# Kernel optimization log

Measured on AMD Instinct MI355X. Metric: run time of the kernel, lower is better.

## Reference

```python
import jax, jax.numpy as jnp
import numpy as np

N_NODES = 100000
N_EDGES = 1700000
NFEAT, NHID1, NHID2, NCLASS = 256, 128, 64, 200


def _deg_inv_sqrt(idx, n):
    deg = jax.ops.segment_sum(jnp.ones(idx.shape[0], jnp.float32), idx, num_segments=n)
    return jnp.power(jnp.clip(deg, 1.0), -0.5)


def _graph_conv(x, W, b, src, dst, n):
    # DGL GraphConv norm='both': D_out^{-1/2} A D_in^{-1/2} X W + b
    # transform first (in_feats >= out_feats), then normalized aggregation
    h = x @ W                                   # [N, out]
    h = h * _deg_inv_sqrt(src, n)[:, None]      # source (out-degree) norm
    m = jax.ops.segment_sum(h[src], dst, num_segments=n)  # SpMM aggregate
    m = m * _deg_inv_sqrt(dst, n)[:, None]      # dest (in-degree) norm
    return m + b


def setup_inputs() -> dict:
    key = jax.random.key(0)
    ks = jax.random.split(key, 9)
    x = jax.random.normal(ks[0], (N_NODES, NFEAT), jnp.float32)
    src = jax.random.randint(ks[1], (N_EDGES,), 0, N_NODES, jnp.int64)
    dst = jax.random.randint(ks[2], (N_EDGES,), 0, N_NODES, jnp.int64)
    def glorot(k, fan_in, fan_out):
        s = jnp.sqrt(6.0 / (fan_in + fan_out))
        return jax.random.uniform(k, (fan_in, fan_out), jnp.float32, -s, s)
    return {
        "x": x, "src": src, "dst": dst,
        "W1": glorot(ks[3], NFEAT, NHID1), "b1": jnp.zeros((NHID1,), jnp.float32),
        "W2": glorot(ks[4], NHID1, NHID2), "b2": jnp.zeros((NHID2,), jnp.float32),
        "Wf": glorot(ks[5], NHID2, NCLASS), "bf": jnp.zeros((NCLASS,), jnp.float32),
    }


def reference(x, src, dst, W1, b1, W2, b2, Wf, bf):
    n = x.shape[0]
    h = jax.nn.relu(_graph_conv(x, W1, b1, src, dst, n))
    # dropout is identity in eval mode (training=False)
    h = jax.nn.relu(_graph_conv(h, W2, b2, src, dst, n))
    logits = h @ Wf + bf
    return jax.nn.log_softmax(logits, axis=1)
```

## Files before the change

kernel.cpp:

```cpp
#include <hip/hip_runtime.h>
#include <math.h>

#define N_NODES 100000
#define N_EDGES 1700000
#define F0 256
#define F1 128
#define F2 64
#define NCLS 200
#define NFPAD 208
#define CAP 64

typedef short bf16x8 __attribute__((ext_vector_type(8)));
typedef float f32x4 __attribute__((ext_vector_type(4)));

__device__ __forceinline__ unsigned short f2bf(float f) {
  unsigned u = __float_as_uint(f);
  return (unsigned short)((u + 0x7FFFu + ((u >> 16) & 1u)) >> 16);
}
__device__ __forceinline__ float bflo(unsigned u) { return __uint_as_float(u << 16); }
__device__ __forceinline__ float bfhi(unsigned u) { return __uint_as_float(u & 0xFFFF0000u); }

__global__ __launch_bounds__(256) void k_dinv(const unsigned* __restrict__ cs,
                                              const unsigned* __restrict__ cnt,
                                              float* __restrict__ dsrc,
                                              float* __restrict__ ddst) {
  int i = blockIdx.x * 256 + threadIdx.x;
  if (i < N_NODES) {
    dsrc[i] = rsqrtf((float)max(cs[i], 1u));
    ddst[i] = rsqrtf((float)max(cnt[i], 1u));
  }
}

__global__ __launch_bounds__(256) void k_castw(const float* __restrict__ W,
                                               unsigned short* __restrict__ Wt,
                                               int K, int N) {
  int idx = blockIdx.x * 256 + threadIdx.x;
  if (idx < K * N) {
    int n = idx / K, k = idx % K;
    Wt[idx] = f2bf(W[(size_t)k * N + n]);
  }
}

__global__ __launch_bounds__(256) void k_castwf(const float* __restrict__ Wf,
                                                unsigned short* __restrict__ Wfp) {
  int idx = blockIdx.x * 256 + threadIdx.x;
  if (idx < NFPAD * F2) {
    int n = idx / F2, k = idx % F2;
    Wfp[idx] = (n < NCLS) ? f2bf(Wf[(size_t)k * NCLS + n]) : (unsigned short)0;
  }
}

__global__ __launch_bounds__(256) void k_fill_gemm1(const int* __restrict__ src,
                                                    const int* __restrict__ dst,
                                                    unsigned* __restrict__ cs,
                                                    unsigned* __restrict__ cnt,
                                                    int* __restrict__ bucket,
                                                    const float* __restrict__ X,
                                                    const unsigned short* __restrict__ Wt,
                                                    unsigned short* __restrict__ out) {
  constexpr int BM = 128;
  constexpr int BK = 64;
  constexpr int LDR = BK + 8;
  constexpr int NB_GEMM = (N_NODES + BM - 1) / BM;
  constexpr int NB_FILL = 2048;
  constexpr int TOT = NB_GEMM + NB_FILL;

  __shared__ unsigned short as[BM][LDR];
  __shared__ unsigned short bs[F1][LDR];

  const int bid = blockIdx.x;
  const int g0 = (int)(((long long)bid * NB_GEMM) / TOT);
  const int g1 = (int)(((long long)(bid + 1) * NB_GEMM) / TOT);

  if (g1 > g0) {
    const int tid = threadIdx.x;
    const int lane = tid & 63;
    const int wid = tid >> 6;
    const int wr = wid >> 1;
    const int wc = wid & 1;
    const int row0 = wr * 64;
    const int col0 = wc * 64;
    const int fq = lane >> 4;
    const int fr = lane & 15;
    const int brow0 = g0 * BM;

    f32x4 acc[4][4];
#pragma unroll
    for (int m = 0; m < 4; ++m)
#pragma unroll
      for (int n = 0; n < 4; ++n) acc[m][n] = (f32x4)(0.f);

    for (int k0 = 0; k0 < F0; k0 += BK) {
      __syncthreads();
      for (int chunk = tid; chunk < BM * (BK / 8); chunk += 256) {
        int r = chunk >> 3, c = chunk & 7;
        int gr = brow0 + r;
        float4 v0 = make_float4(0.f, 0.f, 0.f, 0.f), v1 = v0;
        if (gr < N_NODES) {
          const float* p = X + (size_t)gr * F0 + k0 + c * 8;
          v0 = *(const float4*)p;
          v1 = *(const float4*)(p + 4);
        }
        bf16x8 o;
        o[0] = (short)f2bf(v0.x); o[1] = (short)f2bf(v0.y);
        o[2] = (short)f2bf(v0.z); o[3] = (short)f2bf(v0.w);
        o[4] = (short)f2bf(v1.x); o[5] = (short)f2bf(v1.y);
        o[6] = (short)f2bf(v1.z); o[7] = (short)f2bf(v1.w);
        *(bf16x8*)&as[r][c * 8] = o;
      }
      for (int chunk = tid; chunk < F1 * (BK / 8); chunk += 256) {
        int r = chunk >> 3, c = chunk & 7;
        *(uint4*)&bs[r][c * 8] = *(const uint4*)(Wt + (size_t)r * F0 + k0 + c * 8);
      }
      __syncthreads();
#pragma unroll
      for (int ks = 0; ks < 2; ++ks) {
        bf16x8 af[4], bfv[4];
#pragma unroll
        for (int m = 0; m < 4; ++m)
          af[m] = *(const bf16x8*)&as[row0 + m * 16 + fr][ks * 32 + fq * 8];
#pragma unroll
        for (int n = 0; n < 4; ++n)
          bfv[n] = *(const bf16x8*)&bs[col0 + n * 16 + fr][ks * 32 + fq * 8];
#pragma unroll
        for (int m = 0; m < 4; ++m)
#pragma unroll
          for (int n = 0; n < 4; ++n)
            acc[m][n] = __builtin_amdgcn_mfma_f32_16x16x32_bf16(af[m], bfv[n], acc[m][n], 0, 0, 0);
      }
    }
#pragma unroll
    for (int m = 0; m < 4; ++m) {
#pragma unroll
      for (int j = 0; j < 4; ++j) {
        int grow = brow0 + row0 + m * 16 + fq * 4 + j;
        if (grow < N_NODES) {
#pragma unroll
          for (int n = 0; n < 4; ++n) {
            int col = col0 + n * 16 + fr;
            out[(size_t)grow * F1 + col] = f2bf(acc[m][n][j]);
          }
        }
      }
    }
  } else {
    const int fb = bid - g0;
    int i = fb * 256 + threadIdx.x;
    for (int e = i; e < N_EDGES; e += NB_FILL * 256) {
      int s = src[e], d = dst[e];
      unsigned p = atomicAdd(&cnt[d], 1u);
      if (p < CAP) bucket[d * CAP + p] = s;
      atomicAdd(&cs[s], 1u);
    }
  }
}

template <int K, int BN>
__global__ void k_gemm_mfma(const unsigned short* __restrict__ X,
                            const unsigned short* __restrict__ Wt,
                            const float* __restrict__ scale,
                            unsigned short* __restrict__ out) {
  constexpr int BM = 128;
  constexpr int BK = 64;
  constexpr int LDR = BK + 8;
  constexpr int NWAVE = 2 * (BN / 64);
  constexpr int NTHR = NWAVE * 64;
  __shared__ unsigned short as[BM][LDR];
  __shared__ unsigned short bs[BN][LDR];

  const int tid = threadIdx.x;
  const int lane = tid & 63;
  const int wid = tid >> 6;
  constexpr int WCOLS = BN / 64;
  const int wr = wid / WCOLS;
  const int wc = wid % WCOLS;
  const int row0 = wr * 64;
  const int col0 = wc * 64;
  const int fq = lane >> 4;
  const int fr = lane & 15;
  const int brow0 = blockIdx.x * BM;

  f32x4 acc[4][4];
#pragma unroll
  for (int m = 0; m < 4; ++m)
#pragma unroll
    for (int n = 0; n < 4; ++n) acc[m][n] = (f32x4)(0.f);

  for (int k0 = 0; k0 < K; k0 += BK) {
    __syncthreads();
    for (int chunk = tid; chunk < BM * (BK / 8); chunk += NTHR) {
      int r = chunk >> 3, c = chunk & 7;
      int gr = brow0 + r;
      uint4 v = make_uint4(0u, 0u, 0u, 0u);
      if (gr < N_NODES) v = *(const uint4*)(X + (size_t)gr * K + k0 + c * 8);
      *(uint4*)&as[r][c * 8] = v;
    }
    for (int chunk = tid; chunk < BN * (BK / 8); chunk += NTHR) {
      int r = chunk >> 3, c = chunk & 7;
      *(uint4*)&bs[r][c * 8] = *(const uint4*)(Wt + (size_t)r * K + k0 + c * 8);
    }
    __syncthreads();
#pragma unroll
    for (int ks = 0; ks < 2; ++ks) {
      bf16x8 af[4], bfv[4];
#pragma unroll
      for (int m = 0; m < 4; ++m)
        af[m] = *(const bf16x8*)&as[row0 + m * 16 + fr][ks * 32 + fq * 8];
#pragma unroll
      for (int n = 0; n < 4; ++n)
        bfv[n] = *(const bf16x8*)&bs[col0 + n * 16 + fr][ks * 32 + fq * 8];
#pragma unroll
      for (int m = 0; m < 4; ++m)
#pragma unroll
        for (int n = 0; n < 4; ++n)
          acc[m][n] = __builtin_amdgcn_mfma_f32_16x16x32_bf16(af[m], bfv[n], acc[m][n], 0, 0, 0);
    }
  }

#pragma unroll
  for (int m = 0; m < 4; ++m) {
#pragma unroll
    for (int j = 0; j < 4; ++j) {
      int grow = brow0 + row0 + m * 16 + fq * 4 + j;
      if (grow < N_NODES) {
        float sc = scale[grow];
#pragma unroll
        for (int n = 0; n < 4; ++n) {
          int col = col0 + n * 16 + fr;
          out[(size_t)grow * BN + col] = f2bf(acc[m][n][j] * sc);
        }
      }
    }
  }
}

__global__ __launch_bounds__(256) void k_gather128(const int* __restrict__ bucket,
                                                   const unsigned* __restrict__ cnt,
                                                   const unsigned short* __restrict__ h,
                                                   const float* __restrict__ dsrc,
                                                   const float* __restrict__ ddst,
                                                   const float* __restrict__ b,
                                                   unsigned short* __restrict__ out) {
  const int lane = threadIdx.x & 63;
  const int node = blockIdx.x * 4 + (threadIdx.x >> 6);
  if (node >= N_NODES) return;
  const unsigned deg = min(cnt[node], (unsigned)CAP);
  const int* bp = bucket + (size_t)node * CAP;
  int bidx = (lane < (int)deg) ? bp[lane] : 0;
  float dsv = dsrc[bidx];
  const unsigned* hp = (const unsigned*)h;
  float a0 = 0.f, a1 = 0.f;
  int j = 0;
  for (; j + 4 <= (int)deg; j += 4) {
    int s0 = __shfl(bidx, j + 0), s1 = __shfl(bidx, j + 1);
    int s2 = __shfl(bidx, j + 2), s3 = __shfl(bidx, j + 3);
    float d0 = __shfl(dsv, j + 0), d1 = __shfl(dsv, j + 1);
    float d2 = __shfl(dsv, j + 2), d3 = __shfl(dsv, j + 3);
    unsigned u0 = hp[(size_t)s0 * 64 + lane];
    unsigned u1 = hp[(size_t)s1 * 64 + lane];
    unsigned u2 = hp[(size_t)s2 * 64 + lane];
    unsigned u3 = hp[(size_t)s3 * 64 + lane];
    a0 += d0 * bflo(u0) + d1 * bflo(u1) + d2 * bflo(u2) + d3 * bflo(u3);
    a1 += d0 * bfhi(u0) + d1 * bfhi(u1) + d2 * bfhi(u2) + d3 * bfhi(u3);
  }
  for (; j < (int)deg; ++j) {
    int s = __shfl(bidx, j);
    float ds = __shfl(dsv, j);
    unsigned u = hp[(size_t)s * 64 + lane];
    a0 += ds * bflo(u);
    a1 += ds * bfhi(u);
  }
  float dd = ddst[node];
  float2 bb = *(const float2*)(b + lane * 2);
  float v0 = fmaxf(a0 * dd + bb.x, 0.f);
  float v1 = fmaxf(a1 * dd + bb.y, 0.f);
  unsigned o = (unsigned)f2bf(v0) | ((unsigned)f2bf(v1) << 16);
  ((unsigned*)out)[(size_t)node * 64 + lane] = o;
}

__global__ __launch_bounds__(256) void k_gather64(const int* __restrict__ bucket,
                                                  const unsigned* __restrict__ cnt,
                                                  const unsigned short* __restrict__ h,
                                                  const float* __restrict__ ddst,
                                                  const float* __restrict__ b,
                                                  unsigned short* __restrict__ out) {
  const int lane = threadIdx.x & 63;
  const int node = blockIdx.x * 4 + (threadIdx.x >> 6);
  if (node >= N_NODES) return;
  const int half = lane >> 5;
  const int fl = lane & 31;
  const unsigned deg = min(cnt[node], (unsigned)CAP);
  const int* bp = bucket + (size_t)node * CAP;
  int bidx = (lane < (int)deg) ? bp[lane] : 0;
  const unsigned* hp = (const unsigned*)h;
  float a0 = 0.f, a1 = 0.f;
  int j = half;
  for (; j + 2 < (int)deg; j += 4) {
    int s0 = __shfl(bidx, j), s1 = __shfl(bidx, j + 2);
    unsigned u0 = hp[(size_t)s0 * 32 + fl];
    unsigned u1 = hp[(size_t)s1 * 32 + fl];
    a0 += bflo(u0) + bflo(u1);
    a1 += bfhi(u0) + bfhi(u1);
  }
  if (j < (int)deg) {
    int s = __shfl(bidx, j);
    unsigned u = hp[(size_t)s * 32 + fl];
    a0 += bflo(u);
    a1 += bfhi(u);
  }
  a0 += __shfl_xor(a0, 32);
  a1 += __shfl_xor(a1, 32);
  if (half == 0) {
    float dd = ddst[node];
    float2 bb = *(const float2*)(b + fl * 2);
    float v0 = fmaxf(a0 * dd + bb.x, 0.f);
    float v1 = fmaxf(a1 * dd + bb.y, 0.f);
    unsigned o = (unsigned)f2bf(v0) | ((unsigned)f2bf(v1) << 16);
    ((unsigned*)out)[(size_t)node * 32 + fl] = o;
  }
}

__global__ __launch_bounds__(256) void k_final_mfma(const unsigned short* __restrict__ h,
                                                    const unsigned short* __restrict__ Wfp,
                                                    const float* __restrict__ bf,
                                                    float* __restrict__ out) {
  constexpr int BM = 64;
  constexpr int NF = NFPAD / 16;
  constexpr int LDR = F2 + 8;
  __shared__ unsigned short as[BM][LDR];
  __shared__ unsigned short bs[NFPAD][LDR];

  const int tid = threadIdx.x;
  const int lane = tid & 63;
  const int wid = tid >> 6;
  const int fq = lane >> 4;
  const int fr = lane & 15;
  const int brow0 = blockIdx.x * BM;

  for (int chunk = tid; chunk < BM * 8; chunk += 256) {
    int r = chunk >> 3, c = chunk & 7;
    int gr = brow0 + r;
    uint4 v = make_uint4(0u, 0u, 0u, 0u);
    if (gr < N_NODES) v = *(const uint4*)(h + (size_t)gr * F2 + c * 8);
    *(uint4*)&as[r][c * 8] = v;
  }
  for (int chunk = tid; chunk < NFPAD * 8; chunk += 256) {
    int r = chunk >> 3, c = chunk & 7;
    *(uint4*)&bs[r][c * 8] = *(const uint4*)(Wfp + (size_t)r * F2 + c * 8);
  }
  __syncthreads();

  f32x4 acc[NF];
#pragma unroll
  for (int n = 0; n < NF; ++n) acc[n] = (f32x4)(0.f);

#pragma unroll
  for (int ks = 0; ks < 2; ++ks) {
    bf16x8 af = *(const bf16x8*)&as[wid * 16 + fr][ks * 32 + fq * 8];
#pragma unroll
    for (int n = 0; n < NF; ++n) {
      bf16x8 bv = *(const bf16x8*)&bs[n * 16 + fr][ks * 32 + fq * 8];
      acc[n] = __builtin_amdgcn_mfma_f32_16x16x32_bf16(af, bv, acc[n], 0, 0, 0);
    }
  }

  const int nval = (fr < NCLS - (NF - 1) * 16) ? NF : NF - 1;
  float bias[NF];
#pragma unroll
  for (int n = 0; n < NF; ++n) {
    int col = n * 16 + fr;
    bias[n] = (col < NCLS) ? bf[col] : 0.f;
  }

#pragma unroll
  for (int j = 0; j < 4; ++j) {
    const int grow = brow0 + wid * 16 + fq * 4 + j;
    float v[NF];
    float m = -1e30f;
#pragma unroll
    for (int n = 0; n < NF; ++n) {
      v[n] = acc[n][j] + bias[n];
      if (n < nval) m = fmaxf(m, v[n]);
    }
#pragma unroll
    for (int o = 1; o < 16; o <<= 1) m = fmaxf(m, __shfl_xor(m, o));
    float s = 0.f;
#pragma unroll
    for (int n = 0; n < NF; ++n)
      if (n < nval) s += expf(v[n] - m);
#pragma unroll
    for (int o = 1; o < 16; o <<= 1) s += __shfl_xor(s, o);
    float ls = logf(s);
    if (grow < N_NODES) {
#pragma unroll
      for (int n = 0; n < NF; ++n)
        if (n < nval) out[(size_t)grow * NCLS + n * 16 + fr] = v[n] - m - ls;
    }
  }
}

extern "C" void kernel_launch(void* const* d_in, const int* in_sizes, int n_in,
                              void* d_out, int out_size, void* d_ws, size_t ws_size,
                              hipStream_t stream) {
  const float* x = (const float*)d_in[0];
  const int* src = (const int*)d_in[1];
  const int* dst = (const int*)d_in[2];
  const float* W1 = (const float*)d_in[3];
  const float* b1 = (const float*)d_in[4];
  const float* W2 = (const float*)d_in[5];
  const float* b2 = (const float*)d_in[6];
  const float* Wf = (const float*)d_in[7];
  const float* bf = (const float*)d_in[8];
  float* out = (float*)d_out;

  char* base = (char*)d_ws;
  size_t off = 0;
  auto alloc = [&](size_t bytes) -> void* {
    off = (off + 255) & ~(size_t)255;
    void* p = base + off;
    off += bytes;
    return p;
  };
  unsigned* cs = (unsigned*)alloc(2 * (size_t)N_NODES * 4);
  unsigned* cnt = cs + N_NODES;
  float* dsrc = (float*)alloc(N_NODES * 4);
  float* ddst = (float*)alloc(N_NODES * 4);
  int* bucket = (int*)alloc((size_t)N_NODES * CAP * 4);
  unsigned short* P1 = (unsigned short*)alloc((size_t)N_NODES * F1 * 2);
  unsigned short* P2 = (unsigned short*)alloc((size_t)N_NODES * F1 * 2);
  unsigned short* wt1 = (unsigned short*)alloc((size_t)F1 * F0 * 2);
  unsigned short* wt2 = (unsigned short*)alloc((size_t)F2 * F1 * 2);
  unsigned short* wtf = (unsigned short*)alloc((size_t)NFPAD * F2 * 2);

  unsigned short* h1 = P1;
  unsigned short* h1f = P2;
  unsigned short* h2 = P1;
  unsigned short* agg2 = P2;

  hipMemsetAsync(cs, 0, 2 * (size_t)N_NODES * sizeof(unsigned), stream);

  k_castw<<<(F0 * F1 + 255) / 256, 256, 0, stream>>>(W1, wt1, F0, F1);
  k_castw<<<(F1 * F2 + 255) / 256, 256, 0, stream>>>(W2, wt2, F1, F2);
  k_castwf<<<(NFPAD * F2 + 255) / 256, 256, 0, stream>>>(Wf, wtf);

  constexpr int NB_GEMM = (N_NODES + 127) / 128;
  constexpr int NB_FILL = 2048;
  k_fill_gemm1<<<NB_GEMM + NB_FILL, 256, 0, stream>>>(src, dst, cs, cnt, bucket, x, wt1, h1);

  k_dinv<<<(N_NODES + 255) / 256, 256, 0, stream>>>(cs, cnt, dsrc, ddst);

  k_gather128<<<(N_NODES + 3) / 4, 256, 0, stream>>>(bucket, cnt, h1, dsrc, ddst, b1, h1f);

  k_gemm_mfma<F1, F2><<<(N_NODES + 127) / 128, 128, 0, stream>>>(h1f, wt2, dsrc, h2);
  k_gather64<<<(N_NODES + 3) / 4, 256, 0, stream>>>(bucket, cnt, h2, ddst, b2, agg2);

  k_final_mfma<<<(N_NODES + 63) / 64, 256, 0, stream>>>(agg2, wtf, bf, out);
}
```

Baseline: 340.7 us.

## Merge weight casts, inline degree normalization, and retile layer-2 GEMM

Folds the three weight-cast kernels into one launch and drops the separate degree inverse-sqrt kernel. The gathers and the layer-2 GEMM now compute rsqrt of the raw counts inline. The layer-2 GEMM is replaced by a dedicated kernel with 64-row tiles and two waves, which doubles the block count for better occupancy. This removes two launches and the dsrc/ddst arrays, at the cost of recomputing rsqrt per neighbor and per row, and of a smaller tile with less weight reuse.

```diff
diff --git a/kernel.cpp b/kernel.cpp
--- a/kernel.cpp
+++ b/kernel.cpp
@@ -20,33 +20,24 @@
 __device__ __forceinline__ float bflo(unsigned u) { return __uint_as_float(u << 16); }
 __device__ __forceinline__ float bfhi(unsigned u) { return __uint_as_float(u & 0xFFFF0000u); }
 
-__global__ __launch_bounds__(256) void k_dinv(const unsigned* __restrict__ cs,
-                                              const unsigned* __restrict__ cnt,
-                                              float* __restrict__ dsrc,
-                                              float* __restrict__ ddst) {
-  int i = blockIdx.x * 256 + threadIdx.x;
-  if (i < N_NODES) {
-    dsrc[i] = rsqrtf((float)max(cs[i], 1u));
-    ddst[i] = rsqrtf((float)max(cnt[i], 1u));
-  }
-}
-
-__global__ __launch_bounds__(256) void k_castw(const float* __restrict__ W,
-                                               unsigned short* __restrict__ Wt,
-                                               int K, int N) {
+__global__ __launch_bounds__(256) void k_castall(const float* __restrict__ W1,
+                                                 const float* __restrict__ W2,
+                                                 const float* __restrict__ Wf,
+                                                 unsigned short* __restrict__ wt1,
+                                                 unsigned short* __restrict__ wt2,
+                                                 unsigned short* __restrict__ wtf) {
   int idx = blockIdx.x * 256 + threadIdx.x;
-  if (idx < K * N) {
-    int n = idx / K, k = idx % K;
-    Wt[idx] = f2bf(W[(size_t)k * N + n]);
-  }
-}
-
-__global__ __launch_bounds__(256) void k_castwf(const float* __restrict__ Wf,
-                                                unsigned short* __restrict__ Wfp) {
-  int idx = blockIdx.x * 256 + threadIdx.x;
-  if (idx < NFPAD * F2) {
-    int n = idx / F2, k = idx % F2;
-    Wfp[idx] = (n < NCLS) ? f2bf(Wf[(size_t)k * NCLS + n]) : (unsigned short)0;
+  if (idx < F1 * F0) {
+    int n = idx / F0, k = idx % F0;
+    wt1[idx] = f2bf(W1[(size_t)k * F1 + n]);
+  } else if (idx < F1 * F0 + F2 * F1) {
+    int t = idx - F1 * F0;
+    int n = t / F1, k = t % F1;
+    wt2[t] = f2bf(W2[(size_t)k * F2 + n]);
+  } else if (idx < F1 * F0 + F2 * F1 + NFPAD * F2) {
+    int t = idx - F1 * F0 - F2 * F1;
+    int n = t / F2, k = t % F2;
+    wtf[t] = (n < NCLS) ? f2bf(Wf[(size_t)k * NCLS + n]) : (unsigned short)0;
   }
 }
 
@@ -155,103 +146,24 @@
   }
 }
 
-template <int K, int BN>
-__global__ void k_gemm_mfma(const unsigned short* __restrict__ X,
-                            const unsigned short* __restrict__ Wt,
-                            const float* __restrict__ scale,
-                            unsigned short* __restrict__ out) {
-  constexpr int BM = 128;
-  constexpr int BK = 64;
-  constexpr int LDR = BK + 8;
-  constexpr int NWAVE = 2 * (BN / 64);
-  constexpr int NTHR = NWAVE * 64;
-  __shared__ unsigned short as[BM][LDR];
-  __shared__ unsigned short bs[BN][LDR];
-
-  const int tid = threadIdx.x;
-  const int lane = tid & 63;
-  const int wid = tid >> 6;
-  constexpr int WCOLS = BN / 64;
-  const int wr = wid / WCOLS;
-  const int wc = wid % WCOLS;
-  const int row0 = wr * 64;
-  const int col0 = wc * 64;
-  const int fq = lane >> 4;
-  const int fr = lane & 15;
-  const int brow0 = blockIdx.x * BM;
-
-  f32x4 acc[4][4];
-#pragma unroll
-  for (int m = 0; m < 4; ++m)
-#pragma unroll
-    for (int n = 0; n < 4; ++n) acc[m][n] = (f32x4)(0.f);
-
-  for (int k0 = 0; k0 < K; k0 += BK) {
-    __syncthreads();
-    for (int chunk = tid; chunk < BM * (BK / 8); chunk += NTHR) {
-      int r = chunk >> 3, c = chunk & 7;
-      int gr = brow0 + r;
-      uint4 v = make_uint4(0u, 0u, 0u, 0u);
-      if (gr < N_NODES) v = *(const uint4*)(X + (size_t)gr * K + k0 + c * 8);
-      *(uint4*)&as[r][c * 8] = v;
-    }
-    for (int chunk = tid; chunk < BN * (BK / 8); chunk += NTHR) {
-      int r = chunk >> 3, c = chunk & 7;
-      *(uint4*)&bs[r][c * 8] = *(const uint4*)(Wt + (size_t)r * K + k0 + c * 8);
-    }
-    __syncthreads();
-#pragma unroll
-    for (int ks = 0; ks < 2; ++ks) {
-      bf16x8 af[4], bfv[4];
-#pragma unroll
-      for (int m = 0; m < 4; ++m)
-        af[m] = *(const bf16x8*)&as[row0 + m * 16 + fr][ks * 32 + fq * 8];
-#pragma unroll
-      for (int n = 0; n < 4; ++n)
-        bfv[n] = *(const bf16x8*)&bs[col0 + n * 16 + fr][ks * 32 + fq * 8];
-#pragma unroll
-      for (int m = 0; m < 4; ++m)
-#pragma unroll
-        for (int n = 0; n < 4; ++n)
-          acc[m][n] = __builtin_amdgcn_mfma_f32_16x16x32_bf16(af[m], bfv[n], acc[m][n], 0, 0, 0);
-    }
-  }
-
-#pragma unroll
-  for (int m = 0; m < 4; ++m) {
-#pragma unroll
-    for (int j = 0; j < 4; ++j) {
-      int grow = brow0 + row0 + m * 16 + fq * 4 + j;
-      if (grow < N_NODES) {
-        float sc = scale[grow];
-#pragma unroll
-        for (int n = 0; n < 4; ++n) {
-          int col = col0 + n * 16 + fr;
-          out[(size_t)grow * BN + col] = f2bf(acc[m][n][j] * sc);
-        }
-      }
-    }
-  }
-}
-
 __global__ __launch_bounds__(256) void k_gather128(const int* __restrict__ bucket,
+                                                   const unsigned* __restrict__ cs,
                                                    const unsigned* __restrict__ cnt,
                                                    const unsigned short* __restrict__ h,
-                                                   const float* __restrict__ dsrc,
-                                                   const float* __restrict__ ddst,
                                                    const float* __restrict__ b,
                                                    unsigned short* __restrict__ out) {
   const int lane = threadIdx.x & 63;
   const int node = blockIdx.x * 4 + (threadIdx.x >> 6);
   if (node >= N_NODES) return;
-  const unsigned deg = min(cnt[node], (unsigned)CAP);
+  const unsigned craw = cnt[node];
+  const int deg = (int)min(craw, (unsigned)CAP);
   const int* bp = bucket + (size_t)node * CAP;
-  int bidx = (lane < (int)deg) ? bp[lane] : 0;
-  float dsv = dsrc[bidx];
+  int bidx = (lane < deg) ? bp[lane] : 0;
+  float dsv = rsqrtf((float)max(cs[bidx], 1u));
   const unsigned* hp = (const unsigned*)h;
   float a0 = 0.f, a1 = 0.f;
   int j = 0;
-  for (; j + 4 <= (int)deg; j += 4) {
+  for (; j + 4 <= deg; j += 4) {
     int s0 = __shfl(bidx, j + 0), s1 = __shfl(bidx, j + 1);
     int s2 = __shfl(bidx, j + 2), s3 = __shfl(bidx, j + 3);
     float d0 = __shfl(dsv, j + 0), d1 = __shfl(dsv, j + 1);
@@ -263,14 +175,14 @@
     a0 += d0 * bflo(u0) + d1 * bflo(u1) + d2 * bflo(u2) + d3 * bflo(u3);
     a1 += d0 * bfhi(u0) + d1 * bfhi(u1) + d2 * bfhi(u2) + d3 * bfhi(u3);
   }
-  for (; j < (int)deg; ++j) {
+  for (; j < deg; ++j) {
     int s = __shfl(bidx, j);
     float ds = __shfl(dsv, j);
     unsigned u = hp[(size_t)s * 64 + lane];
     a0 += ds * bflo(u);
     a1 += ds * bfhi(u);
   }
-  float dd = ddst[node];
+  float dd = rsqrtf((float)max(craw, 1u));
   float2 bb = *(const float2*)(b + lane * 2);
   float v0 = fmaxf(a0 * dd + bb.x, 0.f);
   float v1 = fmaxf(a1 * dd + bb.y, 0.f);
@@ -278,10 +190,81 @@
   ((unsigned*)out)[(size_t)node * 64 + lane] = o;
 }
 
+__global__ __launch_bounds__(128) void k_gemm2(const unsigned short* __restrict__ X,
+                                               const unsigned short* __restrict__ Wt,
+                                               const unsigned* __restrict__ cs,
+                                               unsigned short* __restrict__ out) {
+  constexpr int BM = 64;
+  constexpr int BK = 64;
+  constexpr int LDR = BK + 8;
+  __shared__ unsigned short as[BM][LDR];
+  __shared__ unsigned short bs[F2][LDR];
+
+  const int tid = threadIdx.x;
+  const int lane = tid & 63;
+  const int wid = tid >> 6;
+  const int row0 = wid * 32;
+  const int fq = lane >> 4;
+  const int fr = lane & 15;
+  const int brow0 = blockIdx.x * BM;
+
+  f32x4 acc[2][4];
+#pragma unroll
+  for (int m = 0; m < 2; ++m)
+#pragma unroll
+    for (int n = 0; n < 4; ++n) acc[m][n] = (f32x4)(0.f);
+
+  for (int k0 = 0; k0 < F1; k0 += BK) {
+    __syncthreads();
+    for (int chunk = tid; chunk < BM * (BK / 8); chunk += 128) {
+      int r = chunk >> 3, c = chunk & 7;
+      int gr = brow0 + r;
+      uint4 v = make_uint4(0u, 0u, 0u, 0u);
+      if (gr < N_NODES) v = *(const uint4*)(X + (size_t)gr * F1 + k0 + c * 8);
+      *(uint4*)&as[r][c * 8] = v;
+    }
+    for (int chunk = tid; chunk < F2 * (BK / 8); chunk += 128) {
+      int r = chunk >> 3, c = chunk & 7;
+      *(uint4*)&bs[r][c * 8] = *(const uint4*)(Wt + (size_t)r * F1 + k0 + c * 8);
+    }
+    __syncthreads();
+#pragma unroll
+    for (int ks = 0; ks < 2; ++ks) {
+      bf16x8 af[2], bfv[4];
+#pragma unroll
+      for (int m = 0; m < 2; ++m)
+        af[m] = *(const bf16x8*)&as[row0 + m * 16 + fr][ks * 32 + fq * 8];
+#pragma unroll
+      for (int n = 0; n < 4; ++n)
+        bfv[n] = *(const bf16x8*)&bs[n * 16 + fr][ks * 32 + fq * 8];
+#pragma unroll
+      for (int m = 0; m < 2; ++m)
+#pragma unroll
+        for (int n = 0; n < 4; ++n)
+          acc[m][n] = __builtin_amdgcn_mfma_f32_16x16x32_bf16(af[m], bfv[n], acc[m][n], 0, 0, 0);
+    }
+  }
+
+#pragma unroll
+  for (int m = 0; m < 2; ++m) {
+#pragma unroll
+    for (int j = 0; j < 4; ++j) {
+      int grow = brow0 + row0 + m * 16 + fq * 4 + j;
+      if (grow < N_NODES) {
+        float sc = rsqrtf((float)max(cs[grow], 1u));
+#pragma unroll
+        for (int n = 0; n < 4; ++n) {
+          int col = n * 16 + fr;
+          out[(size_t)grow * F2 + col] = f2bf(acc[m][n][j] * sc);
+        }
+      }
+    }
+  }
+}
+
 __global__ __launch_bounds__(256) void k_gather64(const int* __restrict__ bucket,
                                                   const unsigned* __restrict__ cnt,
                                                   const unsigned short* __restrict__ h,
-                                                  const float* __restrict__ ddst,
                                                   const float* __restrict__ b,
                                                   unsigned short* __restrict__ out) {
   const int lane = threadIdx.x & 63;
@@ -289,20 +272,21 @@
   if (node >= N_NODES) return;
   const int half = lane >> 5;
   const int fl = lane & 31;
-  const unsigned deg = min(cnt[node], (unsigned)CAP);
+  const unsigned craw = cnt[node];
+  const int deg = (int)min(craw, (unsigned)CAP);
   const int* bp = bucket + (size_t)node * CAP;
-  int bidx = (lane < (int)deg) ? bp[lane] : 0;
+  int bidx = (lane < deg) ? bp[lane] : 0;
   const unsigned* hp = (const unsigned*)h;
   float a0 = 0.f, a1 = 0.f;
   int j = half;
-  for (; j + 2 < (int)deg; j += 4) {
+  for (; j + 2 < deg; j += 4) {
     int s0 = __shfl(bidx, j), s1 = __shfl(bidx, j + 2);
     unsigned u0 = hp[(size_t)s0 * 32 + fl];
     unsigned u1 = hp[(size_t)s1 * 32 + fl];
     a0 += bflo(u0) + bflo(u1);
     a1 += bfhi(u0) + bfhi(u1);
   }
-  if (j < (int)deg) {
+  if (j < deg) {
     int s = __shfl(bidx, j);
     unsigned u = hp[(size_t)s * 32 + fl];
     a0 += bflo(u);
@@ -311,7 +295,7 @@
   a0 += __shfl_xor(a0, 32);
   a1 += __shfl_xor(a1, 32);
   if (half == 0) {
-    float dd = ddst[node];
+    float dd = rsqrtf((float)max(craw, 1u));
     float2 bb = *(const float2*)(b + fl * 2);
     float v0 = fmaxf(a0 * dd + bb.x, 0.f);
     float v1 = fmaxf(a1 * dd + bb.y, 0.f);
@@ -423,8 +407,6 @@
   };
   unsigned* cs = (unsigned*)alloc(2 * (size_t)N_NODES * 4);
   unsigned* cnt = cs + N_NODES;
-  float* dsrc = (float*)alloc(N_NODES * 4);
-  float* ddst = (float*)alloc(N_NODES * 4);
   int* bucket = (int*)alloc((size_t)N_NODES * CAP * 4);
   unsigned short* P1 = (unsigned short*)alloc((size_t)N_NODES * F1 * 2);
   unsigned short* P2 = (unsigned short*)alloc((size_t)N_NODES * F1 * 2);
@@ -439,20 +421,18 @@
 
   hipMemsetAsync(cs, 0, 2 * (size_t)N_NODES * sizeof(unsigned), stream);
 
-  k_castw<<<(F0 * F1 + 255) / 256, 256, 0, stream>>>(W1, wt1, F0, F1);
-  k_castw<<<(F1 * F2 + 255) / 256, 256, 0, stream>>>(W2, wt2, F1, F2);
-  k_castwf<<<(NFPAD * F2 + 255) / 256, 256, 0, stream>>>(Wf, wtf);
+  constexpr int CAST_TOTAL = F1 * F0 + F2 * F1 + NFPAD * F2;
+  k_castall<<<(CAST_TOTAL + 255) / 256, 256, 0, stream>>>(W1, W2, Wf, wt1, wt2, wtf);
 
   constexpr int NB_GEMM = (N_NODES + 127) / 128;
   constexpr int NB_FILL = 2048;
   k_fill_gemm1<<<NB_GEMM + NB_FILL, 256, 0, stream>>>(src, dst, cs, cnt, bucket, x, wt1, h1);
 
-  k_dinv<<<(N_NODES + 255) / 256, 256, 0, stream>>>(cs, cnt, dsrc, ddst);
-
-  k_gather128<<<(N_NODES + 3) / 4, 256, 0, stream>>>(bucket, cnt, h1, dsrc, ddst, b1, h1f);
-
-  k_gemm_mfma<F1, F2><<<(N_NODES + 127) / 128, 128, 0, stream>>>(h1f, wt2, dsrc, h2);
-  k_gather64<<<(N_NODES + 3) / 4, 256, 0, stream>>>(bucket, cnt, h2, ddst, b2, agg2);
+  k_gather128<<<(N_NODES + 3) / 4, 256, 0, stream>>>(bucket, cs, cnt, h1, b1, h1f);
+
+  k_gemm2<<<(N_NODES + 63) / 64, 128, 0, stream>>>(h1f, wt2, cs, h2);
+
+  k_gather64<<<(N_NODES + 3) / 4, 256, 0, stream>>>(bucket, cnt, h2, b2, agg2);
 
   k_final_mfma<<<(N_NODES + 63) / 64, 256, 0, stream>>>(agg2, wtf, bf, out);
 }
```

New measurement: 327.9 us. 1.04x faster.
